# Optimization experiments

Measured on AMD Instinct MI355X. Metric: run time of the kernel, lower is better.

## Reference

```python
import jax, jax.numpy as jnp
import numpy as np

B, S, H = 1, 2048, 2048
HQ, HKV, D = 16, 4, 128
E, I, TOPK = 16, 768, 2
EPS = 1e-6
ROPE_THETA = 10000.0


def setup_inputs() -> dict:
    key = jax.random.key(0)
    ks = jax.random.split(key, 13)
    s = lambda *sh: 0.02
    return {
        'hidden_states': jax.random.normal(ks[0], (B, S, H), jnp.float32),
        'wq': jax.random.normal(ks[1], (H, HQ * D), jnp.float32) * 0.02,
        'wk': jax.random.normal(ks[2], (H, HKV * D), jnp.float32) * 0.02,
        'wv': jax.random.normal(ks[3], (H, HKV * D), jnp.float32) * 0.02,
        'wo': jax.random.normal(ks[4], (HQ * D, H), jnp.float32) * 0.02,
        'q_scale': jnp.ones((D,), jnp.float32),
        'k_scale': jnp.ones((D,), jnp.float32),
        'router_w': jax.random.normal(ks[5], (H, E), jnp.float32) * 0.02,
        'w_up': jax.random.normal(ks[6], (E, H, I), jnp.float32) * 0.02,
        'b_up': jnp.zeros((E, I), jnp.float32),
        'w_down': jax.random.normal(ks[7], (E, I, H), jnp.float32) * 0.02,
        'b_down': jnp.zeros((E, H), jnp.float32),
    }


def _rmsnorm(x, scale, eps=EPS):
    var = jnp.mean(jnp.square(x), axis=-1, keepdims=True)
    return x * jax.lax.rsqrt(var + eps) * scale


def _rope(x, pos):
    # x: [B, S, nH, D]; rotate-half RoPE
    half = D // 2
    inv_freq = 1.0 / (ROPE_THETA ** (jnp.arange(0, D, 2, dtype=jnp.float32) / D))
    ang = pos[:, None].astype(jnp.float32) * inv_freq[None, :]        # [S, D/2]
    cos = jnp.concatenate([jnp.cos(ang), jnp.cos(ang)], -1)[None, :, None, :]
    sin = jnp.concatenate([jnp.sin(ang), jnp.sin(ang)], -1)[None, :, None, :]
    x1, x2 = x[..., :half], x[..., half:]
    rot = jnp.concatenate([-x2, x1], -1)
    return x * cos + rot * sin


def _attention(x, wq, wk, wv, wo, q_scale, k_scale):
    b, s, _ = x.shape
    pos = jnp.arange(s)
    q = x.reshape(b * s, H) @ wq
    k = x.reshape(b * s, H) @ wk
    v = x.reshape(b * s, H) @ wv
    q = _rmsnorm(q.reshape(b, s, HQ, D), q_scale)
    k = _rmsnorm(k.reshape(b, s, HKV, D), k_scale)
    v = v.reshape(b, s, HKV, D)
    q = _rope(q, pos)
    k = _rope(k, pos)
    rep = HQ // HKV
    k = jnp.repeat(k, rep, axis=2)  # [B, S, HQ, D]
    v = jnp.repeat(v, rep, axis=2)
    scores = jnp.einsum('bqhd,bkhd->bhqk', q, k) / np.sqrt(D).astype(np.float32)
    causal = pos[:, None] >= pos[None, :]
    scores = jnp.where(causal[None, None], scores, jnp.finfo(scores.dtype).min)
    probs = jax.nn.softmax(scores, axis=-1)
    out = jnp.einsum('bhqk,bkhd->bqhd', probs, v).reshape(b, s, HQ * D)
    return out @ wo


def _moe(h, router_w, w_up, b_up, w_down, b_down):
    b, s, hd = h.shape
    x = h.reshape(b * s, hd)                              # [T, H]
    router_logits = x @ router_w                          # [T, E]
    routing_weights = jax.nn.softmax(router_logits, -1)
    _, sel = jax.lax.top_k(routing_weights, TOPK)         # [T, K]
    # one-hot mask summed over k -> 0/1 per (token, expert); note: source
    # multiplies by this MASK, not by the routing weights (faithful quirk).
    mask = jnp.sum(jax.nn.one_hot(sel, E, dtype=x.dtype), axis=1)  # [T, E]
    up = jax.nn.silu(jnp.einsum('th,ehi->eti', x, w_up) + b_up[:, None, :])
    down = jnp.einsum('eti,eih->eth', up, w_down) + b_down[:, None, :]
    out = jnp.einsum('eth,te->th', down, mask)
    return out.reshape(b, s, hd), router_logits


def reference(hidden_states, wq, wk, wv, wo, q_scale, k_scale,
              router_w, w_up, b_up, w_down, b_down):
    attn_out = _attention(hidden_states, wq, wk, wv, wo, q_scale, k_scale)
    h = hidden_states + attn_out
    moe_out, router_logits = _moe(h, router_w, w_up, b_up, w_down, b_down)
    return h + moe_out, router_logits
```

## Files before the change

### kernel.cpp

```cpp
#include <hip/hip_runtime.h>
#include <math.h>

#define SEQ 2048
#define HDIM 2048
#define NHQ 16
#define NHKV 4
#define DH 128
#define NE 16
#define NI 768
#define EPSV 1e-6f
#define QKVS 3072
#define MOE_TILES 48

typedef __attribute__((ext_vector_type(8))) __bf16 bf16x8;
typedef __attribute__((ext_vector_type(4))) float f32x4;
typedef unsigned short ushort_t;

__device__ __forceinline__ ushort_t f2bf(float f) {
    union { float f; unsigned int u; } v; v.f = f;
    unsigned int u = v.u;
    unsigned int r = (u + 0x7FFFu + ((u >> 16) & 1u)) >> 16;
    return (ushort_t)r;
}
__device__ __forceinline__ float bf2f(ushort_t b) {
    union { unsigned int u; float f; } v; v.u = ((unsigned int)b) << 16;
    return v.f;
}
__device__ __forceinline__ void async16(const ushort_t* g, ushort_t* l) {
    __builtin_amdgcn_global_load_lds(
        (const __attribute__((address_space(1))) void*)g,
        (__attribute__((address_space(3))) void*)l, 16, 0, 0);
}

__global__ void split_cvt(const float* __restrict__ in, ushort_t* __restrict__ hi,
                          ushort_t* __restrict__ lo) {
    int i = blockIdx.x * 256 + threadIdx.x;
    float4 v = ((const float4*)in)[i];
    ushort_t h0 = f2bf(v.x), h1 = f2bf(v.y), h2 = f2bf(v.z), h3 = f2bf(v.w);
    ushort4 h = make_ushort4(h0, h1, h2, h3);
    ushort4 l = make_ushort4(f2bf(v.x - bf2f(h0)), f2bf(v.y - bf2f(h1)),
                             f2bf(v.z - bf2f(h2)), f2bf(v.w - bf2f(h3)));
    ((ushort4*)hi)[i] = h;
    ((ushort4*)lo)[i] = l;
}

__global__ void transpose_split(const float* __restrict__ in, ushort_t* __restrict__ hi,
                                ushort_t* __restrict__ lo, int K, int N) {
    __shared__ float tls[32][33];
    int tx = threadIdx.x & 31, ty = threadIdx.x >> 5;
    size_t k0 = (size_t)blockIdx.y * 32, n0 = (size_t)blockIdx.x * 32;
    #pragma unroll
    for (int i = 0; i < 32; i += 8) tls[ty + i][tx] = in[(k0 + ty + i) * N + n0 + tx];
    __syncthreads();
    #pragma unroll
    for (int i = 0; i < 32; i += 8) {
        float v = tls[tx][ty + i];
        ushort_t h = f2bf(v);
        size_t o = (n0 + ty + i) * K + k0 + tx;
        hi[o] = h;
        lo[o] = f2bf(v - bf2f(h));
    }
}

__global__ void transpose_cvt(const float* __restrict__ in, ushort_t* __restrict__ out,
                              int K, int N) {
    const float* ib = in + (size_t)blockIdx.z * K * N;
    ushort_t* ob = out + (size_t)blockIdx.z * K * N;
    __shared__ float tls[32][33];
    int tx = threadIdx.x & 31, ty = threadIdx.x >> 5;
    size_t k0 = (size_t)blockIdx.y * 32, n0 = (size_t)blockIdx.x * 32;
    #pragma unroll
    for (int i = 0; i < 32; i += 8) tls[ty + i][tx] = ib[(k0 + ty + i) * N + n0 + tx];
    __syncthreads();
    #pragma unroll
    for (int i = 0; i < 32; i += 8)
        ob[(n0 + ty + i) * K + k0 + tx] = f2bf(tls[tx][ty + i]);
}

__global__ void vT_split(const float* __restrict__ qkv, ushort_t* __restrict__ vth,
                         ushort_t* __restrict__ vtl) {
    __shared__ float tls[32][33];
    int tx = threadIdx.x & 31, ty = threadIdx.x >> 5;
    int kvh = blockIdx.z;
    size_t s0 = (size_t)blockIdx.x * 32;
    size_t d0 = (size_t)blockIdx.y * 32;
    #pragma unroll
    for (int i = 0; i < 32; i += 8)
        tls[ty + i][tx] = qkv[(s0 + ty + i) * QKVS + 2560 + (size_t)kvh * DH + d0 + tx];
    __syncthreads();
    #pragma unroll
    for (int i = 0; i < 32; i += 8) {
        float v = tls[tx][ty + i];
        ushort_t hh = f2bf(v);
        size_t o = ((size_t)kvh * DH + d0 + ty + i) * SEQ + s0 + tx;
        vth[o] = hh;
        vtl[o] = f2bf(v - bf2f(hh));
    }
}

#define BM 128
#define BN 128
#define BK 32
__global__ __launch_bounds__(256, 2)
void gemm_split(const ushort_t* __restrict__ Ahi, const ushort_t* __restrict__ Alo,
                const ushort_t* __restrict__ Bhi, const ushort_t* __restrict__ Blo,
                float* __restrict__ C, int ldc,
                const float* __restrict__ R, ushort_t* __restrict__ Cbf,
                int N, int K) {
    __shared__ ushort_t sAh[BM * BK], sAl[BM * BK], sBh[BN * BK], sBl[BN * BK];
    const int tid = threadIdx.x;
    const int wave = tid >> 6, lane = tid & 63;
    const int wy = wave >> 1, wx = wave & 1;
    const int quad = lane >> 4, m16 = lane & 15;
    const size_t rowBase = (size_t)blockIdx.y * BM;
    const size_t colBase = (size_t)blockIdx.x * BN;
    const int srow = wave * 32 + (lane >> 2);
    const int scol = (lane & 3) * 8;
    const size_t aoff0 = (rowBase + srow) * K + scol;
    const size_t aoff1 = aoff0 + (size_t)16 * K;
    const size_t boff0 = (colBase + srow) * K + scol;
    const size_t boff1 = boff0 + (size_t)16 * K;
    ushort_t* dA0 = &sAh[(wave * 32) * BK];
    ushort_t* dA1 = &sAh[(wave * 32 + 16) * BK];
    ushort_t* dAl0 = &sAl[(wave * 32) * BK];
    ushort_t* dAl1 = &sAl[(wave * 32 + 16) * BK];
    ushort_t* dB0 = &sBh[(wave * 32) * BK];
    ushort_t* dB1 = &sBh[(wave * 32 + 16) * BK];
    ushort_t* dBl0 = &sBl[(wave * 32) * BK];
    ushort_t* dBl1 = &sBl[(wave * 32 + 16) * BK];
    f32x4 acc[4][4] = {};
    for (int k0 = 0; k0 < K; k0 += BK) {
        __syncthreads();
        async16(Ahi + aoff0 + k0, dA0);
        async16(Ahi + aoff1 + k0, dA1);
        async16(Alo + aoff0 + k0, dAl0);
        async16(Alo + aoff1 + k0, dAl1);
        async16(Bhi + boff0 + k0, dB0);
        async16(Bhi + boff1 + k0, dB1);
        async16(Blo + boff0 + k0, dBl0);
        async16(Blo + boff1 + k0, dBl1);
        __syncthreads();
        bf16x8 ah[4], al[4], bh[4], bl[4];
        #pragma unroll
        for (int i = 0; i < 4; i++) {
            ah[i] = *(const bf16x8*)&sAh[(wy * 64 + i * 16 + m16) * BK + quad * 8];
            al[i] = *(const bf16x8*)&sAl[(wy * 64 + i * 16 + m16) * BK + quad * 8];
        }
        #pragma unroll
        for (int j = 0; j < 4; j++) {
            bh[j] = *(const bf16x8*)&sBh[(wx * 64 + j * 16 + m16) * BK + quad * 8];
            bl[j] = *(const bf16x8*)&sBl[(wx * 64 + j * 16 + m16) * BK + quad * 8];
        }
        #pragma unroll
        for (int i = 0; i < 4; i++)
            #pragma unroll
            for (int j = 0; j < 4; j++) {
                acc[i][j] = __builtin_amdgcn_mfma_f32_16x16x32_bf16(ah[i], bh[j], acc[i][j], 0, 0, 0);
                acc[i][j] = __builtin_amdgcn_mfma_f32_16x16x32_bf16(ah[i], bl[j], acc[i][j], 0, 0, 0);
                acc[i][j] = __builtin_amdgcn_mfma_f32_16x16x32_bf16(al[i], bh[j], acc[i][j], 0, 0, 0);
            }
    }
    #pragma unroll
    for (int i = 0; i < 4; i++)
        #pragma unroll
        for (int j = 0; j < 4; j++)
            #pragma unroll
            for (int r = 0; r < 4; r++) {
                size_t row = rowBase + wy * 64 + i * 16 + quad * 4 + r;
                size_t col = colBase + wx * 64 + j * 16 + m16;
                float v = acc[i][j][r];
                if (R) v += R[row * N + col];
                C[row * ldc + col] = v;
                if (Cbf) Cbf[row * N + col] = f2bf(v);
            }
}

__global__ void norm_rope(const float* __restrict__ qkv, const float* __restrict__ q_scale,
                          const float* __restrict__ k_scale,
                          ushort_t* __restrict__ qh, ushort_t* __restrict__ ql,
                          ushort_t* __restrict__ kh, ushort_t* __restrict__ kl) {
    const int s = blockIdx.x;
    const int h = blockIdx.y;
    const int t = threadIdx.x;
    const float* ptr;
    const float* scale;
    if (h < NHQ) { ptr = qkv + (size_t)s * QKVS + h * DH; scale = q_scale; }
    else         { ptr = qkv + (size_t)s * QKVS + 2048 + (h - NHQ) * DH; scale = k_scale; }
    __shared__ float sh[DH];
    __shared__ float red[128];
    float x = ptr[t];
    red[t] = x * x;
    __syncthreads();
    #pragma unroll
    for (int off = 64; off > 0; off >>= 1) {
        if (t < off) red[t] += red[t + off];
        __syncthreads();
    }
    float var = red[0] * (1.0f / DH);
    float r = rsqrtf(var + EPSV);
    float xn = x * r * scale[t];
    sh[t] = xn;
    __syncthreads();
    int i = t & 63;
    float inv_freq = exp2f(-(float)i * 0.20762050593046014f);
    float ang = (float)s * inv_freq;
    float c = cosf(ang), sn = sinf(ang);
    float y;
    if (t < 64) y = xn * c - sh[t + 64] * sn;
    else        y = xn * c + sh[t - 64] * sn;
    ushort_t yh = f2bf(y);
    ushort_t yl = f2bf(y - bf2f(yh));
    if (h < NHQ) {
        size_t o = ((size_t)h * SEQ + s) * DH + t;
        qh[o] = yh; ql[o] = yl;
    } else {
        size_t o = ((size_t)(h - NHQ) * SEQ + s) * DH + t;
        kh[o] = yh; kl[o] = yl;
    }
}

#define AQT 64
#define AKT 64
__global__ __launch_bounds__(256, 2)
void attn_flash(const ushort_t* __restrict__ qh_b, const ushort_t* __restrict__ ql_b,
                const ushort_t* __restrict__ kh_b, const ushort_t* __restrict__ kl_b,
                const ushort_t* __restrict__ vth_b, const ushort_t* __restrict__ vtl_b,
                ushort_t* __restrict__ ohi, ushort_t* __restrict__ olo) {
    const int by = blockIdx.y;
    const int bx = blockIdx.x;
    const int qb = (by < 8) ? bx : (31 - bx);
    const int h = by;
    const int kvh = h >> 2;
    const int r0 = qb * AQT;
    const int tid = threadIdx.x;
    const int wave = tid >> 6, lane = tid & 63;
    const int quad = lane >> 4, m16 = lane & 15;

    __shared__ ushort_t sKh[AKT * DH], sKl[AKT * DH];
    __shared__ ushort_t sVh[DH * AKT], sVl[DH * AKT];
    __shared__ ushort_t sPh[4 * 16 * AKT], sPl[4 * 16 * AKT];

    bf16x8 qfh[4], qfl[4];
    {
        const size_t qrow = ((size_t)h * SEQ + r0 + wave * 16 + m16) * DH;
        #pragma unroll
        for (int kk = 0; kk < 4; kk++) {
            qfh[kk] = *(const bf16x8*)&qh_b[qrow + kk * 32 + quad * 8];
            qfl[kk] = *(const bf16x8*)&ql_b[qrow + kk * 32 + quad * 8];
        }
    }

    f32x4 accO[8] = {};
    float mrow[4], lrow[4];
    #pragma unroll
    for (int r = 0; r < 4; r++) { mrow[r] = -3.0e38f; lrow[r] = 0.f; }

    const float scl = 0.08838834764831845f;
    const int nkt = qb + 1;

    for (int kt = 0; kt < nkt; kt++) {
        __syncthreads();
        #pragma unroll
        for (int i = 0; i < 4; i++) {
            int seg = i * 4 + wave;
            int row = seg * 4 + (lane >> 4);
            int clog = (lane & 15) ^ (row & 7);
            size_t gk = ((size_t)kvh * SEQ + kt * AKT + row) * DH + clog * 8;
            async16(kh_b + gk, &sKh[seg * 512]);
            async16(kl_b + gk, &sKl[seg * 512]);
        }
        #pragma unroll
        for (int i = 0; i < 4; i++) {
            int seg = i * 4 + wave;
            int row = seg * 8 + (lane >> 3);
            int clog = (lane & 7) ^ (row & 7);
            size_t gv = ((size_t)kvh * DH + row) * SEQ + kt * AKT + clog * 8;
            async16(vth_b + gv, &sVh[seg * 512]);
            async16(vtl_b + gv, &sVl[seg * 512]);
        }
        __syncthreads();

        f32x4 accS[4] = {};
        #pragma unroll
        for (int kk = 0; kk < 4; kk++) {
            #pragma unroll
            for (int j = 0; j < 4; j++) {
                int n = j * 16 + m16;
                int c = (kk * 4 + quad) ^ (n & 7);
                bf16x8 bh = *(const bf16x8*)&sKh[n * 128 + c * 8];
                bf16x8 bl = *(const bf16x8*)&sKl[n * 128 + c * 8];
                accS[j] = __builtin_amdgcn_mfma_f32_16x16x32_bf16(qfh[kk], bh, accS[j], 0, 0, 0);
                accS[j] = __builtin_amdgcn_mfma_f32_16x16x32_bf16(qfl[kk], bh, accS[j], 0, 0, 0);
                accS[j] = __builtin_amdgcn_mfma_f32_16x16x32_bf16(qfh[kk], bl, accS[j], 0, 0, 0);
            }
        }

        const int diag = (kt == qb);
        float tmax[4];
        #pragma unroll
        for (int r = 0; r < 4; r++) tmax[r] = -3.0e38f;
        #pragma unroll
        for (int j = 0; j < 4; j++)
            #pragma unroll
            for (int r = 0; r < 4; r++) {
                float s = accS[j][r] * scl;
                if (diag) {
                    int ra = wave * 16 + quad * 4 + r;
                    int ca = j * 16 + m16;
                    if (ca > ra) s = -3.0e38f;
                }
                accS[j][r] = s;
                tmax[r] = fmaxf(tmax[r], s);
            }
        #pragma unroll
        for (int r = 0; r < 4; r++) {
            #pragma unroll
            for (int w = 1; w < 16; w <<= 1)
                tmax[r] = fmaxf(tmax[r], __shfl_xor(tmax[r], w));
            float newm = fmaxf(mrow[r], tmax[r]);
            float alpha = __expf(mrow[r] - newm);
            mrow[r] = newm;
            float psum = 0.f;
            #pragma unroll
            for (int j = 0; j < 4; j++) {
                float p = __expf(accS[j][r] - newm);
                accS[j][r] = p;
                psum += p;
            }
            #pragma unroll
            for (int w = 1; w < 16; w <<= 1) psum += __shfl_xor(psum, w);
            lrow[r] = lrow[r] * alpha + psum;
            #pragma unroll
            for (int j2 = 0; j2 < 8; j2++) accO[j2][r] *= alpha;
        }

        #pragma unroll
        for (int j = 0; j < 4; j++)
            #pragma unroll
            for (int r = 0; r < 4; r++) {
                int pr = quad * 4 + r;
                int cb = j * 32 + m16 * 2;
                int sw = (cb ^ ((pr & 7) << 4)) >> 1;
                float p = accS[j][r];
                ushort_t ph = f2bf(p);
                sPh[wave * 1024 + pr * 64 + sw] = ph;
                sPl[wave * 1024 + pr * 64 + sw] = f2bf(p - bf2f(ph));
            }
        __syncthreads();

        #pragma unroll
        for (int kk2 = 0; kk2 < 2; kk2++) {
            int cpa = (kk2 * 4 + quad) ^ (m16 & 7);
            bf16x8 pah = *(const bf16x8*)&sPh[wave * 1024 + m16 * 64 + cpa * 8];
            bf16x8 pal = *(const bf16x8*)&sPl[wave * 1024 + m16 * 64 + cpa * 8];
            #pragma unroll
            for (int j2 = 0; j2 < 8; j2++) {
                int n = j2 * 16 + m16;
                int c = (kk2 * 4 + quad) ^ (n & 7);
                bf16x8 vh = *(const bf16x8*)&sVh[n * 64 + c * 8];
                bf16x8 vl = *(const bf16x8*)&sVl[n * 64 + c * 8];
                accO[j2] = __builtin_amdgcn_mfma_f32_16x16x32_bf16(pah, vh, accO[j2], 0, 0, 0);
                accO[j2] = __builtin_amdgcn_mfma_f32_16x16x32_bf16(pal, vh, accO[j2], 0, 0, 0);
                accO[j2] = __builtin_amdgcn_mfma_f32_16x16x32_bf16(pah, vl, accO[j2], 0, 0, 0);
            }
        }
    }

    #pragma unroll
    for (int r = 0; r < 4; r++) {
        float inv = 1.0f / lrow[r];
        size_t ra = (size_t)r0 + wave * 16 + quad * 4 + r;
        #pragma unroll
        for (int j2 = 0; j2 < 8; j2++) {
            float val = accO[j2][r] * inv;
            size_t o = ra * (NHQ * DH) + (size_t)h * DH + j2 * 16 + m16;
            ushort_t hh = f2bf(val);
            ohi[o] = hh;
            olo[o] = f2bf(val - bf2f(hh));
        }
    }
}

__global__ void router_topk(const float* __restrict__ hbuf, const float* __restrict__ rw,
                            float* __restrict__ logits_out, int* __restrict__ cnt,
                            int* __restrict__ plist) {
    const int tok = blockIdx.x;
    const int tid = threadIdx.x;
    __shared__ float part[256];
    const int e = tid & 15, chunk = tid >> 4;
    const float* hr = hbuf + (size_t)tok * HDIM;
    float sum = 0.f;
    const int k0 = chunk * 128;
    for (int x = k0; x < k0 + 128; x++) sum += hr[x] * rw[(size_t)x * NE + e];
    part[tid] = sum;
    __syncthreads();
    if (tid < 16) {
        float s = 0.f;
        #pragma unroll
        for (int c = 0; c < 16; c++) s += part[c * 16 + tid];
        part[tid] = s;
    }
    __syncthreads();
    if (tid == 0) {
        float best = -1e30f; int bi = 0;
        for (int e2 = 0; e2 < 16; e2++) if (part[e2] > best) { best = part[e2]; bi = e2; }
        float best2 = -1e30f; int bi2 = 0;
        for (int e2 = 0; e2 < 16; e2++) if (e2 != bi && part[e2] > best2) { best2 = part[e2]; bi2 = e2; }
        int p0 = atomicAdd(&cnt[bi], 1);
        plist[bi * SEQ + p0] = tok * 2;
        int p1 = atomicAdd(&cnt[bi2], 1);
        plist[bi2 * SEQ + p1] = tok * 2 + 1;
    }
    if (tid < 16) logits_out[(size_t)tok * NE + tid] = part[tid];
}

__global__ void tilemap(const int* __restrict__ cnt, int* __restrict__ te,
                        int* __restrict__ to, int* __restrict__ ntiles) {
    if (threadIdx.x == 0 && blockIdx.x == 0) {
        int n = 0;
        for (int e = 0; e < NE; e++) {
            int c = cnt[e];
            for (int off = 0; off < c; off += BM) { te[n] = e; to[n] = off; n++; }
        }
        *ntiles = n;
    }
}

__global__ __launch_bounds__(256, 2)
void moe_up_mfma(const ushort_t* __restrict__ hbf, const int* __restrict__ plist,
                 const int* __restrict__ cnt, const int* __restrict__ te,
                 const int* __restrict__ to, const int* __restrict__ nt,
                 const ushort_t* __restrict__ wupt, const float* __restrict__ b_up,
                 ushort_t* __restrict__ U) {
    const int t = blockIdx.y;
    if (t >= *nt) return;
    const int ex = te[t], r0 = to[t], cnt_e = cnt[ex];
    __shared__ int sp[BM];
    __shared__ ushort_t sA[BM * BK], sB[BN * BK];
    const int tid = threadIdx.x;
    if (tid < BM) {
        int idx = r0 + tid;
        sp[tid] = (idx < cnt_e) ? plist[ex * SEQ + idx] : 0;
    }
    __syncthreads();
    const int wave = tid >> 6, lane = tid & 63;
    const int wy = wave >> 1, wx = wave & 1;
    const int quad = lane >> 4, m16 = lane & 15;
    const int srow = wave * 32 + (lane >> 2);
    const int scol = (lane & 3) * 8;
    const int p0 = sp[srow], p1 = sp[srow + 16];
    const ushort_t* Ag0 = hbf + (size_t)(p0 >> 1) * HDIM + scol;
    const ushort_t* Ag1 = hbf + (size_t)(p1 >> 1) * HDIM + scol;
    const size_t colBase = (size_t)blockIdx.x * BN;
    const ushort_t* Bt = wupt + (size_t)ex * HDIM * NI;
    const ushort_t* Bg0 = Bt + (colBase + srow) * HDIM + scol;
    const ushort_t* Bg1 = Bg0 + (size_t)16 * HDIM;
    ushort_t* dA0 = &sA[(wave * 32) * BK];
    ushort_t* dA1 = &sA[(wave * 32 + 16) * BK];
    ushort_t* dB0 = &sB[(wave * 32) * BK];
    ushort_t* dB1 = &sB[(wave * 32 + 16) * BK];
    f32x4 acc[4][4] = {};
    for (int k0 = 0; k0 < HDIM; k0 += BK) {
        __syncthreads();
        async16(Ag0 + k0, dA0);
        async16(Ag1 + k0, dA1);
        async16(Bg0 + k0, dB0);
        async16(Bg1 + k0, dB1);
        __syncthreads();
        bf16x8 af[4], bfr[4];
        #pragma unroll
        for (int i = 0; i < 4; i++)
            af[i] = *(const bf16x8*)&sA[(wy * 64 + i * 16 + m16) * BK + quad * 8];
        #pragma unroll
        for (int j = 0; j < 4; j++)
            bfr[j] = *(const bf16x8*)&sB[(wx * 64 + j * 16 + m16) * BK + quad * 8];
        #pragma unroll
        for (int i = 0; i < 4; i++)
            #pragma unroll
            for (int j = 0; j < 4; j++)
                acc[i][j] = __builtin_amdgcn_mfma_f32_16x16x32_bf16(af[i], bfr[j], acc[i][j], 0, 0, 0);
    }
    #pragma unroll
    for (int i = 0; i < 4; i++)
        #pragma unroll
        for (int j = 0; j < 4; j++)
            #pragma unroll
            for (int r = 0; r < 4; r++) {
                int rl = wy * 64 + i * 16 + quad * 4 + r;
                if (r0 + rl < cnt_e) {
                    int p = sp[rl];
                    size_t col = colBase + wx * 64 + j * 16 + m16;
                    float x = acc[i][j][r] + b_up[(size_t)ex * NI + col];
                    U[(size_t)p * NI + col] = f2bf(x / (1.0f + __expf(-x)));
                }
            }
}

__global__ __launch_bounds__(256, 2)
void moe_down_mfma(const ushort_t* __restrict__ U, const int* __restrict__ plist,
                   const int* __restrict__ cnt, const int* __restrict__ te,
                   const int* __restrict__ to, const int* __restrict__ nt,
                   const ushort_t* __restrict__ wdnt, const float* __restrict__ b_down,
                   float* __restrict__ hout) {
    const int t = blockIdx.y;
    if (t >= *nt) return;
    const int ex = te[t], r0 = to[t], cnt_e = cnt[ex];
    __shared__ int sp[BM];
    __shared__ ushort_t sA[BM * BK], sB[BN * BK];
    const int tid = threadIdx.x;
    if (tid < BM) {
        int idx = r0 + tid;
        sp[tid] = (idx < cnt_e) ? plist[ex * SEQ + idx] : 0;
    }
    __syncthreads();
    const int wave = tid >> 6, lane = tid & 63;
    const int wy = wave >> 1, wx = wave & 1;
    const int quad = lane >> 4, m16 = lane & 15;
    const int srow = wave * 32 + (lane >> 2);
    const int scol = (lane & 3) * 8;
    const int p0 = sp[srow], p1 = sp[srow + 16];
    const ushort_t* Ag0 = U + (size_t)p0 * NI + scol;
    const ushort_t* Ag1 = U + (size_t)p1 * NI + scol;
    const size_t colBase = (size_t)blockIdx.x * BN;
    const ushort_t* Bt = wdnt + (size_t)ex * NI * HDIM;
    const ushort_t* Bg0 = Bt + (colBase + srow) * NI + scol;
    const ushort_t* Bg1 = Bg0 + (size_t)16 * NI;
    ushort_t* dA0 = &sA[(wave * 32) * BK];
    ushort_t* dA1 = &sA[(wave * 32 + 16) * BK];
    ushort_t* dB0 = &sB[(wave * 32) * BK];
    ushort_t* dB1 = &sB[(wave * 32 + 16) * BK];
    f32x4 acc[4][4] = {};
    for (int k0 = 0; k0 < NI; k0 += BK) {
        __syncthreads();
        async16(Ag0 + k0, dA0);
        async16(Ag1 + k0, dA1);
        async16(Bg0 + k0, dB0);
        async16(Bg1 + k0, dB1);
        __syncthreads();
        bf16x8 af[4], bfr[4];
        #pragma unroll
        for (int i = 0; i < 4; i++)
            af[i] = *(const bf16x8*)&sA[(wy * 64 + i * 16 + m16) * BK + quad * 8];
        #pragma unroll
        for (int j = 0; j < 4; j++)
            bfr[j] = *(const bf16x8*)&sB[(wx * 64 + j * 16 + m16) * BK + quad * 8];
        #pragma unroll
        for (int i = 0; i < 4; i++)
            #pragma unroll
            for (int j = 0; j < 4; j++)
                acc[i][j] = __builtin_amdgcn_mfma_f32_16x16x32_bf16(af[i], bfr[j], acc[i][j], 0, 0, 0);
    }
    #pragma unroll
    for (int i = 0; i < 4; i++)
        #pragma unroll
        for (int j = 0; j < 4; j++)
            #pragma unroll
            for (int r = 0; r < 4; r++) {
                int rl = wy * 64 + i * 16 + quad * 4 + r;
                if (r0 + rl < cnt_e) {
                    int tok = sp[rl] >> 1;
                    size_t col = colBase + wx * 64 + j * 16 + m16;
                    float v = acc[i][j][r] + b_down[(size_t)ex * HDIM + col];
                    atomicAdd(&hout[(size_t)tok * HDIM + col], v);
                }
            }
}

extern "C" void kernel_launch(void* const* d_in, const int* in_sizes, int n_in,
                              void* d_out, int out_size, void* d_ws, size_t ws_size,
                              hipStream_t stream) {
    (void)in_sizes; (void)n_in; (void)out_size; (void)ws_size;
    const float* hidden   = (const float*)d_in[0];
    const float* wq       = (const float*)d_in[1];
    const float* wk       = (const float*)d_in[2];
    const float* wv       = (const float*)d_in[3];
    const float* wo       = (const float*)d_in[4];
    const float* q_scale  = (const float*)d_in[5];
    const float* k_scale  = (const float*)d_in[6];
    const float* router_w = (const float*)d_in[7];
    const float* w_up     = (const float*)d_in[8];
    const float* b_up     = (const float*)d_in[9];
    const float* w_down   = (const float*)d_in[10];
    const float* b_down   = (const float*)d_in[11];

    float* out = (float*)d_out;
    float* h_out      = out;
    float* logits_out = out + (size_t)SEQ * HDIM;

    ushort_t* pool = (ushort_t*)d_ws;
    ushort_t* hid_hi  = pool;
    ushort_t* hid_lo  = hid_hi + (size_t)4194304;
    ushort_t* wqkv_hi = hid_lo + (size_t)4194304;
    ushort_t* wqkv_lo = wqkv_hi + (size_t)6291456;
    float*    qkv     = (float*)(wqkv_lo + (size_t)6291456);
    ushort_t* attn_hi = (ushort_t*)(qkv + (size_t)6291456);
    ushort_t* attn_lo = attn_hi + (size_t)4194304;
    ushort_t* wo_hi   = attn_lo + (size_t)4194304;
    ushort_t* wo_lo   = wo_hi + (size_t)4194304;

    ushort_t* qsp_h = hid_hi;
    ushort_t* qsp_l = hid_lo;
    ushort_t* ksp_h = wqkv_hi;
    ushort_t* ksp_l = wqkv_hi + (size_t)1048576;
    ushort_t* vt_h  = wqkv_hi + (size_t)2097152;
    ushort_t* vt_l  = wqkv_hi + (size_t)3145728;

    ushort_t* w_up_t  = pool;
    ushort_t* w_dn_t  = w_up_t + (size_t)25165824;
    ushort_t* U_ws    = w_dn_t + (size_t)25165824;

    ushort_t* hbf     = pool + (size_t)53477376;
    int* cnt_ws   = (int*)(hbf + (size_t)4194304);
    int* plist_ws = cnt_ws + 16;
    int* te_ws    = plist_ws + NE * SEQ;
    int* to_ws    = te_ws + 64;
    int* nt_ws    = to_ws + 64;

    split_cvt<<<dim3(4096), 256, 0, stream>>>(hidden, hid_hi, hid_lo);
    transpose_split<<<dim3(64, 64), 256, 0, stream>>>(wq, wqkv_hi, wqkv_lo, HDIM, 2048);
    transpose_split<<<dim3(16, 64), 256, 0, stream>>>(wk, wqkv_hi + (size_t)2048 * HDIM,
                                                      wqkv_lo + (size_t)2048 * HDIM, HDIM, 512);
    transpose_split<<<dim3(16, 64), 256, 0, stream>>>(wv, wqkv_hi + (size_t)2560 * HDIM,
                                                      wqkv_lo + (size_t)2560 * HDIM, HDIM, 512);
    transpose_split<<<dim3(64, 64), 256, 0, stream>>>(wo, wo_hi, wo_lo, HDIM, HDIM);

    gemm_split<<<dim3(QKVS / BN, SEQ / BM), 256, 0, stream>>>(
        hid_hi, hid_lo, wqkv_hi, wqkv_lo, qkv, QKVS, nullptr, nullptr, QKVS, HDIM);

    norm_rope<<<dim3(SEQ, NHQ + NHKV), 128, 0, stream>>>(qkv, q_scale, k_scale,
                                                         qsp_h, qsp_l, ksp_h, ksp_l);
    vT_split<<<dim3(64, 4, 4), 256, 0, stream>>>(qkv, vt_h, vt_l);

    attn_flash<<<dim3(SEQ / AQT, NHQ), 256, 0, stream>>>(
        qsp_h, qsp_l, ksp_h, ksp_l, vt_h, vt_l, attn_hi, attn_lo);

    gemm_split<<<dim3(HDIM / BN, SEQ / BM), 256, 0, stream>>>(
        attn_hi, attn_lo, wo_hi, wo_lo, h_out, HDIM, hidden, hbf, HDIM, HDIM);

    transpose_cvt<<<dim3(24, 64, 16), 256, 0, stream>>>(w_up, w_up_t, HDIM, NI);
    transpose_cvt<<<dim3(64, 24, 16), 256, 0, stream>>>(w_down, w_dn_t, NI, HDIM);

    hipMemsetAsync(cnt_ws, 0, NE * sizeof(int), stream);
    router_topk<<<dim3(SEQ), 256, 0, stream>>>(h_out, router_w, logits_out, cnt_ws, plist_ws);
    tilemap<<<1, 64, 0, stream>>>(cnt_ws, te_ws, to_ws, nt_ws);

    moe_up_mfma<<<dim3(NI / BN, MOE_TILES), 256, 0, stream>>>(
        hbf, plist_ws, cnt_ws, te_ws, to_ws, nt_ws, w_up_t, b_up, U_ws);
    moe_down_mfma<<<dim3(HDIM / BN, MOE_TILES), 256, 0, stream>>>(
        U_ws, plist_ws, cnt_ws, te_ws, to_ws, nt_ws, w_dn_t, b_down, h_out);
}
```

Before: 810.8 us.

## Read K/V directly from global in flash attention, remap blocks per XCD, vectorize weight transpose

The attention kernel stops staging K and V tiles in LDS and loads MFMA operands straight from global memory. It drops the per-tile barriers and raises the occupancy hint to 3 blocks per SU. Blocks are remapped so heads sharing a KV head land on the same XCD for L2 reuse, and s_setprio wraps the MFMA sections. The MoE weight transpose-convert kernel now uses 64x64 tiles with float4 loads and ushort4 stores to cut memory transactions. The risks are higher global/L2 traffic, uncoalesced strided operand loads, and the loss of the causal-balancing qb reversal in the new block mapping.

```diff
diff --git a/kernel.cpp b/kernel.cpp
--- a/kernel.cpp
+++ b/kernel.cpp
@@ -66,15 +66,27 @@
                               int K, int N) {
     const float* ib = in + (size_t)blockIdx.z * K * N;
     ushort_t* ob = out + (size_t)blockIdx.z * K * N;
-    __shared__ float tls[32][33];
-    int tx = threadIdx.x & 31, ty = threadIdx.x >> 5;
-    size_t k0 = (size_t)blockIdx.y * 32, n0 = (size_t)blockIdx.x * 32;
-    #pragma unroll
-    for (int i = 0; i < 32; i += 8) tls[ty + i][tx] = ib[(k0 + ty + i) * N + n0 + tx];
-    __syncthreads();
-    #pragma unroll
-    for (int i = 0; i < 32; i += 8)
-        ob[(n0 + ty + i) * K + k0 + tx] = f2bf(tls[tx][ty + i]);
+    __shared__ float tls[64][65];
+    int tx = threadIdx.x & 15, ty = threadIdx.x >> 4;
+    size_t k0 = (size_t)blockIdx.y * 64, n0 = (size_t)blockIdx.x * 64;
+    #pragma unroll
+    for (int i = 0; i < 4; i++) {
+        float4 v = *(const float4*)&ib[(k0 + ty + i * 16) * N + n0 + tx * 4];
+        tls[ty + i * 16][tx * 4 + 0] = v.x;
+        tls[ty + i * 16][tx * 4 + 1] = v.y;
+        tls[ty + i * 16][tx * 4 + 2] = v.z;
+        tls[ty + i * 16][tx * 4 + 3] = v.w;
+    }
+    __syncthreads();
+    #pragma unroll
+    for (int i = 0; i < 4; i++) {
+        ushort4 o;
+        o.x = f2bf(tls[tx * 4 + 0][ty + i * 16]);
+        o.y = f2bf(tls[tx * 4 + 1][ty + i * 16]);
+        o.z = f2bf(tls[tx * 4 + 2][ty + i * 16]);
+        o.w = f2bf(tls[tx * 4 + 3][ty + i * 16]);
+        *(ushort4*)&ob[(n0 + ty + i * 16) * K + k0 + tx * 4] = o;
+    }
 }
 
 __global__ void vT_split(const float* __restrict__ qkv, ushort_t* __restrict__ vth,
@@ -221,23 +233,21 @@
 
 #define AQT 64
 #define AKT 64
-__global__ __launch_bounds__(256, 2)
+__global__ __launch_bounds__(256, 3)
 void attn_flash(const ushort_t* __restrict__ qh_b, const ushort_t* __restrict__ ql_b,
                 const ushort_t* __restrict__ kh_b, const ushort_t* __restrict__ kl_b,
                 const ushort_t* __restrict__ vth_b, const ushort_t* __restrict__ vtl_b,
                 ushort_t* __restrict__ ohi, ushort_t* __restrict__ olo) {
-    const int by = blockIdx.y;
-    const int bx = blockIdx.x;
-    const int qb = (by < 8) ? bx : (31 - bx);
-    const int h = by;
-    const int kvh = h >> 2;
+    const int flat = blockIdx.y * 32 + blockIdx.x;
+    const int xcd = flat & 7, w = flat >> 3;
+    const int kvh = xcd >> 1;
+    const int h = kvh * 4 + (xcd & 1) * 2 + (w & 1);
+    const int qb = w >> 1;
     const int r0 = qb * AQT;
     const int tid = threadIdx.x;
     const int wave = tid >> 6, lane = tid & 63;
     const int quad = lane >> 4, m16 = lane & 15;
 
-    __shared__ ushort_t sKh[AKT * DH], sKl[AKT * DH];
-    __shared__ ushort_t sVh[DH * AKT], sVl[DH * AKT];
     __shared__ ushort_t sPh[4 * 16 * AKT], sPl[4 * 16 * AKT];
 
     bf16x8 qfh[4], qfl[4];
@@ -250,6 +260,11 @@
         }
     }
 
+    const ushort_t* Kh = kh_b + (size_t)kvh * SEQ * DH;
+    const ushort_t* Kl = kl_b + (size_t)kvh * SEQ * DH;
+    const ushort_t* Vh = vth_b + (size_t)kvh * DH * SEQ;
+    const ushort_t* Vl = vtl_b + (size_t)kvh * DH * SEQ;
+
     f32x4 accO[8] = {};
     float mrow[4], lrow[4];
     #pragma unroll
@@ -259,41 +274,24 @@
     const int nkt = qb + 1;
 
     for (int kt = 0; kt < nkt; kt++) {
-        __syncthreads();
-        #pragma unroll
-        for (int i = 0; i < 4; i++) {
-            int seg = i * 4 + wave;
-            int row = seg * 4 + (lane >> 4);
-            int clog = (lane & 15) ^ (row & 7);
-            size_t gk = ((size_t)kvh * SEQ + kt * AKT + row) * DH + clog * 8;
-            async16(kh_b + gk, &sKh[seg * 512]);
-            async16(kl_b + gk, &sKl[seg * 512]);
-        }
-        #pragma unroll
-        for (int i = 0; i < 4; i++) {
-            int seg = i * 4 + wave;
-            int row = seg * 8 + (lane >> 3);
-            int clog = (lane & 7) ^ (row & 7);
-            size_t gv = ((size_t)kvh * DH + row) * SEQ + kt * AKT + clog * 8;
-            async16(vth_b + gv, &sVh[seg * 512]);
-            async16(vtl_b + gv, &sVl[seg * 512]);
-        }
-        __syncthreads();
+        const int k0 = kt * AKT;
 
         f32x4 accS[4] = {};
-        #pragma unroll
-        for (int kk = 0; kk < 4; kk++) {
-            #pragma unroll
-            for (int j = 0; j < 4; j++) {
-                int n = j * 16 + m16;
-                int c = (kk * 4 + quad) ^ (n & 7);
-                bf16x8 bh = *(const bf16x8*)&sKh[n * 128 + c * 8];
-                bf16x8 bl = *(const bf16x8*)&sKl[n * 128 + c * 8];
+        __builtin_amdgcn_s_setprio(1);
+        #pragma unroll
+        for (int j = 0; j < 4; j++) {
+            const ushort_t* kp  = Kh + (size_t)(k0 + j * 16 + m16) * DH + quad * 8;
+            const ushort_t* klp = Kl + (size_t)(k0 + j * 16 + m16) * DH + quad * 8;
+            #pragma unroll
+            for (int kk = 0; kk < 4; kk++) {
+                bf16x8 bh = *(const bf16x8*)(kp + kk * 32);
+                bf16x8 bl = *(const bf16x8*)(klp + kk * 32);
                 accS[j] = __builtin_amdgcn_mfma_f32_16x16x32_bf16(qfh[kk], bh, accS[j], 0, 0, 0);
                 accS[j] = __builtin_amdgcn_mfma_f32_16x16x32_bf16(qfl[kk], bh, accS[j], 0, 0, 0);
                 accS[j] = __builtin_amdgcn_mfma_f32_16x16x32_bf16(qfh[kk], bl, accS[j], 0, 0, 0);
             }
         }
+        __builtin_amdgcn_s_setprio(0);
 
         const int diag = (kt == qb);
         float tmax[4];
@@ -315,8 +313,8 @@
         #pragma unroll
         for (int r = 0; r < 4; r++) {
             #pragma unroll
-            for (int w = 1; w < 16; w <<= 1)
-                tmax[r] = fmaxf(tmax[r], __shfl_xor(tmax[r], w));
+            for (int w2 = 1; w2 < 16; w2 <<= 1)
+                tmax[r] = fmaxf(tmax[r], __shfl_xor(tmax[r], w2));
             float newm = fmaxf(mrow[r], tmax[r]);
             float alpha = __expf(mrow[r] - newm);
             mrow[r] = newm;
@@ -328,7 +326,7 @@
                 psum += p;
             }
             #pragma unroll
-            for (int w = 1; w < 16; w <<= 1) psum += __shfl_xor(psum, w);
+            for (int w2 = 1; w2 < 16; w2 <<= 1) psum += __shfl_xor(psum, w2);
             lrow[r] = lrow[r] * alpha + psum;
             #pragma unroll
             for (int j2 = 0; j2 < 8; j2++) accO[j2][r] *= alpha;
@@ -346,8 +344,8 @@
                 sPh[wave * 1024 + pr * 64 + sw] = ph;
                 sPl[wave * 1024 + pr * 64 + sw] = f2bf(p - bf2f(ph));
             }
-        __syncthreads();
-
+
+        __builtin_amdgcn_s_setprio(1);
         #pragma unroll
         for (int kk2 = 0; kk2 < 2; kk2++) {
             int cpa = (kk2 * 4 + quad) ^ (m16 & 7);
@@ -355,15 +353,16 @@
             bf16x8 pal = *(const bf16x8*)&sPl[wave * 1024 + m16 * 64 + cpa * 8];
             #pragma unroll
             for (int j2 = 0; j2 < 8; j2++) {
-                int n = j2 * 16 + m16;
-                int c = (kk2 * 4 + quad) ^ (n & 7);
-                bf16x8 vh = *(const bf16x8*)&sVh[n * 64 + c * 8];
-                bf16x8 vl = *(const bf16x8*)&sVl[n * 64 + c * 8];
+                const ushort_t* vp  = Vh + (size_t)(j2 * 16 + m16) * SEQ + k0 + kk2 * 32 + quad * 8;
+                const ushort_t* vlp = Vl + (size_t)(j2 * 16 + m16) * SEQ + k0 + kk2 * 32 + quad * 8;
+                bf16x8 vh = *(const bf16x8*)vp;
+                bf16x8 vl = *(const bf16x8*)vlp;
                 accO[j2] = __builtin_amdgcn_mfma_f32_16x16x32_bf16(pah, vh, accO[j2], 0, 0, 0);
                 accO[j2] = __builtin_amdgcn_mfma_f32_16x16x32_bf16(pal, vh, accO[j2], 0, 0, 0);
                 accO[j2] = __builtin_amdgcn_mfma_f32_16x16x32_bf16(pah, vl, accO[j2], 0, 0, 0);
             }
         }
+        __builtin_amdgcn_s_setprio(0);
     }
 
     #pragma unroll
@@ -637,8 +636,8 @@
     gemm_split<<<dim3(HDIM / BN, SEQ / BM), 256, 0, stream>>>(
         attn_hi, attn_lo, wo_hi, wo_lo, h_out, HDIM, hidden, hbf, HDIM, HDIM);
 
-    transpose_cvt<<<dim3(24, 64, 16), 256, 0, stream>>>(w_up, w_up_t, HDIM, NI);
-    transpose_cvt<<<dim3(64, 24, 16), 256, 0, stream>>>(w_down, w_dn_t, NI, HDIM);
+    transpose_cvt<<<dim3(NI / 64, HDIM / 64, 16), 256, 0, stream>>>(w_up, w_up_t, HDIM, NI);
+    transpose_cvt<<<dim3(HDIM / 64, NI / 64, 16), 256, 0, stream>>>(w_down, w_dn_t, NI, HDIM);
 
     hipMemsetAsync(cnt_ws, 0, NE * sizeof(int), stream);
     router_topk<<<dim3(SEQ), 256, 0, stream>>>(h_out, router_w, logits_out, cnt_ws, plist_ws);
```

Result: slower. 1.057 ms (+30.4%).
